# Optimization experiments

Measured on AMD Instinct MI355X. Metric: run time of the kernel, lower is better.

## Reference

```python
import jax, jax.numpy as jnp
import numpy as np

B, C, CI, H, W = 4, 128, 64, 64, 64


def conv1x1(x, w, b):
    # x: [B,C,H,W], w: [Cout,Cin], b: [Cout]
    return jnp.einsum('bchw,oc->bohw', x, w) + b[None, :, None, None]


def setup_inputs() -> dict:
    key = jax.random.key(0)
    ks = jax.random.split(key, 10)
    s = 0.05  # keep logits in a sane range for softmax
    return {
        'x0': jax.random.normal(ks[0], (B, C, H, W), jnp.float32),
        'x1': jax.random.normal(ks[1], (B, C, H, W), jnp.float32),
        'g_w': jax.random.normal(ks[2], (CI, C), jnp.float32) * s,
        'g_b': jax.random.normal(ks[3], (CI,), jnp.float32) * s,
        'theta_w': jax.random.normal(ks[4], (CI, C), jnp.float32) * s,
        'theta_b': jax.random.normal(ks[5], (CI,), jnp.float32) * s,
        'phi_w': jax.random.normal(ks[6], (CI, C), jnp.float32) * s,
        'phi_b': jax.random.normal(ks[7], (CI,), jnp.float32) * s,
        'W_w': jax.random.normal(ks[8], (C, CI), jnp.float32) * s,
        'W_b': jax.random.normal(ks[9], (C,), jnp.float32) * s,
    }


def reference(x0, x1, g_w, g_b, theta_w, theta_b, phi_w, phi_b, W_w, W_b):
    b, c, h, w = x0.shape
    n = h * w
    ci = g_w.shape[0]
    g_x = conv1x1(x0, g_w, g_b).reshape(b, ci, n).transpose(0, 2, 1)      # [B,N,Ci]
    theta_x = conv1x1(x1, theta_w, theta_b).reshape(b, ci, n).transpose(0, 2, 1)  # [B,N,Ci]
    phi_x = conv1x1(x0, phi_w, phi_b).reshape(b, ci, n)                    # [B,Ci,N]
    f = jnp.einsum('bqc,bck->bqk', theta_x, phi_x)                         # [B,N,N]
    f_div_C = jax.nn.softmax(f, axis=-1)
    y = jnp.einsum('bqk,bkc->bqc', f_div_C, g_x)                           # [B,N,Ci]
    y = y.transpose(0, 2, 1).reshape(b, ci, h, w)
    W_y = conv1x1(y, W_w, W_b)
    return W_y + x0
```

## Files before the change

### kernel.cpp

```cpp
#include <hip/hip_runtime.h>
#include <hip/hip_bf16.h>


typedef unsigned int   u32;
typedef unsigned short u16;
typedef __attribute__((ext_vector_type(8))) short short8;
typedef __attribute__((ext_vector_type(4))) short short4v;
typedef __attribute__((ext_vector_type(4))) float f32x4;

#define LOG2E 1.4426950408889634f
#define KSPLIT 8

__device__ __forceinline__ float b2f(u16 v) {
  union { u32 u; float f; } x; x.u = ((u32)v) << 16; return x.f;
}
__device__ __forceinline__ u16 f2b(float f) {
  u32 u = __float_as_uint(f);
  return (u16)((u + 0x8000u) >> 16);
}
__device__ __forceinline__ short8 load_w_frag(const float* p, float s) {
  const float4 f0 = ((const float4*)p)[0];
  const float4 f1 = ((const float4*)p)[1];
  union { u32 w[4]; short8 s8; } r;
  r.w[0] = (u32)f2b(f0.x * s) | ((u32)f2b(f0.y * s) << 16);
  r.w[1] = (u32)f2b(f0.z * s) | ((u32)f2b(f0.w * s) << 16);
  r.w[2] = (u32)f2b(f1.x * s) | ((u32)f2b(f1.y * s) << 16);
  r.w[3] = (u32)f2b(f1.z * s) | ((u32)f2b(f1.w * s) << 16);
  return r.s8;
}


__global__ __launch_bounds__(256) void qkv_fused_kernel(
    const float* __restrict__ x0, const float* __restrict__ x1,
    const float* __restrict__ tw, const float* __restrict__ tb,
    const float* __restrict__ pw, const float* __restrict__ pb,
    const float* __restrict__ gw, const float* __restrict__ gb,
    u16* __restrict__ Q, u16* __restrict__ K, u16* __restrict__ Vt)
{
  const int n0 = blockIdx.x * 64;
  const int b  = blockIdx.y;
  const int t  = threadIdx.x;

  __shared__ __align__(16) short xt[2][64][136];

  #pragma unroll 8
  for (int i = 0; i < 64; ++i) {
    const int idx = i * 256 + t;
    const int tensor = idx >> 13;
    const int c = (idx >> 6) & 127;
    const int n = idx & 63;
    const float v = (tensor ? x1 : x0)[((size_t)b * 128 + c) * 4096 + n0 + n];
    xt[tensor][n][c] = (short)f2b(v);
  }
  asm volatile("" ::: "memory");
  __syncthreads();

  const int wave = t >> 6;
  const int lane = t & 63;
  const int quad = lane >> 4, l15 = lane & 15;

  if (wave < 2) {
    const int conv = wave;
    const float* wsrc = conv ? pw : tw;
    const float  ws   = conv ? 1.f : LOG2E;
    const short* xl   = &xt[conv ? 0 : 1][0][0];

    f32x4 acc[4][4];
    #pragma unroll
    for (int i = 0; i < 4; ++i)
      #pragma unroll
      for (int j = 0; j < 4; ++j) acc[i][j] = (f32x4){0.f, 0.f, 0.f, 0.f};

    #pragma unroll
    for (int kk = 0; kk < 4; ++kk) {
      short8 wf[4], xf[4];
      #pragma unroll
      for (int ot = 0; ot < 4; ++ot)
        wf[ot] = load_w_frag(wsrc + (ot * 16 + l15) * 128 + kk * 32 + quad * 8, ws);
      #pragma unroll
      for (int nt = 0; nt < 4; ++nt)
        xf[nt] = *(const short8*)(xl + (nt * 16 + l15) * 136 + kk * 32 + quad * 8);
      #pragma unroll
      for (int i = 0; i < 4; ++i)
        #pragma unroll
        for (int j = 0; j < 4; ++j)
          acc[i][j] = __builtin_amdgcn_mfma_f32_16x16x32_bf16(xf[i], wf[j], acc[i][j], 0, 0, 0);
    }

    u16* dst = (conv ? K : Q) + (size_t)b * 4096 * 64;
    const float* bias = conv ? pb : tb;
    const float bscale = conv ? 1.f : LOG2E;
    #pragma unroll
    for (int ot = 0; ot < 4; ++ot) {
      const float bv = bias[ot * 16 + l15] * bscale;
      #pragma unroll
      for (int nt = 0; nt < 4; ++nt)
        #pragma unroll
        for (int r = 0; r < 4; ++r) {
          const int n = n0 + nt * 16 + quad * 4 + r;
          dst[(size_t)n * 64 + ot * 16 + l15] = f2b(acc[nt][ot][r] + bv);
        }
    }
  } else {
    const int oh = wave - 2;
    const short* xl = &xt[0][0][0];

    f32x4 acc[2][4];
    #pragma unroll
    for (int i = 0; i < 2; ++i)
      #pragma unroll
      for (int j = 0; j < 4; ++j) acc[i][j] = (f32x4){0.f, 0.f, 0.f, 0.f};

    #pragma unroll
    for (int kk = 0; kk < 4; ++kk) {
      short8 wf[2], xf[4];
      #pragma unroll
      for (int ot = 0; ot < 2; ++ot)
        wf[ot] = load_w_frag(gw + ((oh * 2 + ot) * 16 + l15) * 128 + kk * 32 + quad * 8, 1.f);
      #pragma unroll
      for (int nt = 0; nt < 4; ++nt)
        xf[nt] = *(const short8*)(xl + (nt * 16 + l15) * 136 + kk * 32 + quad * 8);
      #pragma unroll
      for (int i = 0; i < 2; ++i)
        #pragma unroll
        for (int j = 0; j < 4; ++j)
          acc[i][j] = __builtin_amdgcn_mfma_f32_16x16x32_bf16(wf[i], xf[j], acc[i][j], 0, 0, 0);
    }

    u16* dst = Vt + (size_t)b * 64 * 4096;
    #pragma unroll
    for (int ot = 0; ot < 2; ++ot)
      #pragma unroll
      for (int r = 0; r < 4; ++r) {
        const int o = (oh * 2 + ot) * 16 + quad * 4 + r;
        const float bv = gb[o];
        #pragma unroll
        for (int nc = 0; nc < 4; ++nc)
          dst[(size_t)o * 4096 + n0 + nc * 16 + l15] = f2b(acc[ot][nc][r] + bv);
      }
  }
}

__global__ __launch_bounds__(256) void attn_kernel(
    const u16* __restrict__ Q, const u16* __restrict__ K,
    const u16* __restrict__ Vt, u16* __restrict__ Opart,
    float* __restrict__ Lp)
{
  const int qt = blockIdx.x, b = blockIdx.y, ks = blockIdx.z;
  const int tid  = threadIdx.x;
  const int wave = tid >> 6;
  const int lane = tid & 63;
  const int quad = lane >> 4;
  const int l15  = lane & 15;

  __shared__ __align__(16) short P_lds[4][64][72];
  short* pw = &P_lds[wave][0][0];

  const int q0 = qt * 256 + wave * 64;
  const u16* Qb = Q  + (size_t)b * 4096 * 64;
  const u16* Kb = K  + (size_t)b * 4096 * 64;
  const u16* Vb = Vt + (size_t)b * 64 * 4096;

  short8 qf[4][2];
  #pragma unroll
  for (int nt = 0; nt < 4; ++nt) {
    const u16* qp = Qb + (size_t)(q0 + nt * 16 + l15) * 64 + quad * 8;
    qf[nt][0] = *(const short8*)qp;
    qf[nt][1] = *(const short8*)(qp + 32);
  }

  f32x4 oacc[4][4];
  #pragma unroll
  for (int i = 0; i < 4; ++i)
    #pragma unroll
    for (int j = 0; j < 4; ++j)
      oacc[i][j] = (f32x4){0.f, 0.f, 0.f, 0.f};
  float lsum[4] = {0.f, 0.f, 0.f, 0.f};

  const int kbase = ks * (4096 / KSPLIT);
  const int NKT   = 4096 / KSPLIT / 64;

  short8 kf[4][2];
  #pragma unroll
  for (int mt = 0; mt < 4; ++mt) {
    const u16* kp = Kb + (size_t)(kbase + mt * 16 + l15) * 64 + quad * 8;
    kf[mt][0] = *(const short8*)kp;
    kf[mt][1] = *(const short8*)(kp + 32);
  }

  for (int kt = 0; kt < NKT; ++kt) {
    const int k0 = kbase + kt * 64;

    short8 vf[4][2];
    #pragma unroll
    for (int nd = 0; nd < 4; ++nd) {
      const u16* vp = Vb + (size_t)(nd * 16 + l15) * 4096 + k0 + quad * 8;
      vf[nd][0] = *(const short8*)vp;
      vf[nd][1] = *(const short8*)(vp + 32);
    }

    #pragma unroll
    for (int mt = 0; mt < 4; ++mt) {
      #pragma unroll
      for (int nt = 0; nt < 4; ++nt) {
        f32x4 s = {0.f, 0.f, 0.f, 0.f};
        s = __builtin_amdgcn_mfma_f32_16x16x32_bf16(kf[mt][0], qf[nt][0], s, 0, 0, 0);
        s = __builtin_amdgcn_mfma_f32_16x16x32_bf16(kf[mt][1], qf[nt][1], s, 0, 0, 0);
        float p0 = exp2f(s[0]), p1 = exp2f(s[1]), p2 = exp2f(s[2]), p3 = exp2f(s[3]);
        lsum[nt] += (p0 + p1) + (p2 + p3);
        u32 u0 = __float_as_uint(p0) + 0x8000u;
        u32 u1 = __float_as_uint(p1) + 0x8000u;
        u32 u2 = __float_as_uint(p2) + 0x8000u;
        u32 u3 = __float_as_uint(p3) + 0x8000u;
        union { uint2 u; short4v s4; } pk;
        pk.u.x = __builtin_amdgcn_perm(u1, u0, 0x07060302u);
        pk.u.y = __builtin_amdgcn_perm(u3, u2, 0x07060302u);
        *(short4v*)(pw + (nt * 16 + l15) * 72 + mt * 16 + quad * 4) = pk.s4;
      }
    }

    if (kt < NKT - 1) {
      #pragma unroll
      for (int mt = 0; mt < 4; ++mt) {
        const u16* kp = Kb + (size_t)(k0 + 64 + mt * 16 + l15) * 64 + quad * 8;
        kf[mt][0] = *(const short8*)kp;
        kf[mt][1] = *(const short8*)(kp + 32);
      }
    }

    asm volatile("" ::: "memory");

    #pragma unroll
    for (int mq = 0; mq < 4; ++mq) {
      const short* pr = pw + (mq * 16 + l15) * 72 + quad * 8;
      short8 pa0 = *(const short8*)pr;
      short8 pa1 = *(const short8*)(pr + 32);
      #pragma unroll
      for (int nd = 0; nd < 4; ++nd) {
        oacc[mq][nd] = __builtin_amdgcn_mfma_f32_16x16x32_bf16(pa0, vf[nd][0], oacc[mq][nd], 0, 0, 0);
        oacc[mq][nd] = __builtin_amdgcn_mfma_f32_16x16x32_bf16(pa1, vf[nd][1], oacc[mq][nd], 0, 0, 0);
      }
    }

    asm volatile("" ::: "memory");
  }

  #pragma unroll
  for (int nt = 0; nt < 4; ++nt) {
    float v = lsum[nt];
    v += __shfl_xor(v, 16, 64);
    v += __shfl_xor(v, 32, 64);
    lsum[nt] = v;
  }
  float* LpB = Lp + ((size_t)ks * 4 + b) * 4096;
  if (quad == 0) {
    #pragma unroll
    for (int nt = 0; nt < 4; ++nt)
      LpB[q0 + nt * 16 + l15] = lsum[nt];
  }

  u16* Ob = Opart + ((size_t)ks * 4 + b) * 4096 * 64;
  #pragma unroll
  for (int mq = 0; mq < 4; ++mq)
    #pragma unroll
    for (int nd = 0; nd < 4; ++nd)
      #pragma unroll
      for (int r = 0; r < 4; ++r) {
        int q = q0 + mq * 16 + quad * 4 + r;
        Ob[(size_t)q * 64 + nd * 16 + l15] = f2b(oacc[mq][nd][r]);
      }
}

__global__ __launch_bounds__(256) void out_fused_kernel(
    const u16* __restrict__ Opart, const float* __restrict__ Lp,
    const float* __restrict__ Wf, const float* __restrict__ Wbf,
    const float* __restrict__ x0, float* __restrict__ out)
{
  const int n0 = blockIdx.x * 64;
  const int b  = blockIdx.y;
  const int t  = threadIdx.x;

  __shared__ __align__(16) short Ys[64][72];

  {
    const int nl = t >> 2;
    const int q4 = t & 3;
    const int ng = n0 + nl;

    float l = 0.f;
    #pragma unroll
    for (int ks = 0; ks < KSPLIT; ++ks)
      l += Lp[((size_t)ks * 4 + b) * 4096 + ng];

    float a[16];
    #pragma unroll
    for (int j = 0; j < 16; ++j) a[j] = 0.f;
    #pragma unroll
    for (int ks = 0; ks < KSPLIT; ++ks) {
      const uint4* row = (const uint4*)(Opart + (((size_t)ks * 4 + b) * 4096 + ng) * 64 + q4 * 16);
      #pragma unroll
      for (int v = 0; v < 2; ++v) {
        uint4 r = row[v];
        u32 wds[4] = {r.x, r.y, r.z, r.w};
        #pragma unroll
        for (int j = 0; j < 4; ++j) {
          a[v * 8 + 2 * j]     += __uint_as_float(wds[j] << 16);
          a[v * 8 + 2 * j + 1] += __uint_as_float(wds[j] & 0xffff0000u);
        }
      }
    }
    const float rinv = 1.f / l;
    union { u32 w[8]; short8 s8[2]; } pk;
    #pragma unroll
    for (int j = 0; j < 8; ++j)
      pk.w[j] = (u32)f2b(a[2 * j] * rinv) | ((u32)f2b(a[2 * j + 1] * rinv) << 16);
    *(short8*)&Ys[nl][q4 * 16]     = pk.s8[0];
    *(short8*)&Ys[nl][q4 * 16 + 8] = pk.s8[1];
  }
  asm volatile("" ::: "memory");
  __syncthreads();

  const int wave = t >> 6;
  const int lane = t & 63;
  const int quad = lane >> 4, l15 = lane & 15;

  f32x4 acc[2][4];
  #pragma unroll
  for (int i = 0; i < 2; ++i)
    #pragma unroll
    for (int j = 0; j < 4; ++j) acc[i][j] = (f32x4){0.f, 0.f, 0.f, 0.f};

  #pragma unroll
  for (int kk = 0; kk < 2; ++kk) {
    short8 wf[2], yf[4];
    #pragma unroll
    for (int ot = 0; ot < 2; ++ot)
      wf[ot] = load_w_frag(Wf + ((wave * 2 + ot) * 16 + l15) * 64 + kk * 32 + quad * 8, 1.f);
    #pragma unroll
    for (int nt = 0; nt < 4; ++nt)
      yf[nt] = *(const short8*)&Ys[nt * 16 + l15][kk * 32 + quad * 8];
    #pragma unroll
    for (int i = 0; i < 2; ++i)
      #pragma unroll
      for (int j = 0; j < 4; ++j)
        acc[i][j] = __builtin_amdgcn_mfma_f32_16x16x32_bf16(wf[i], yf[j], acc[i][j], 0, 0, 0);
  }

  #pragma unroll
  for (int ot = 0; ot < 2; ++ot)
    #pragma unroll
    for (int r = 0; r < 4; ++r) {
      const int o = (wave * 2 + ot) * 16 + quad * 4 + r;
      const float bv = Wbf[o];
      #pragma unroll
      for (int nt = 0; nt < 4; ++nt) {
        const size_t idx = ((size_t)(b * 128 + o)) * 4096 + n0 + nt * 16 + l15;
        out[idx] = acc[ot][nt][r] + bv + x0[idx];
      }
    }
}

extern "C" void kernel_launch(void* const* d_in, const int* in_sizes, int n_in,
                              void* d_out, int out_size, void* d_ws, size_t ws_size,
                              hipStream_t stream) {
  const float* x0 = (const float*)d_in[0];
  const float* x1 = (const float*)d_in[1];
  const float* gw = (const float*)d_in[2];
  const float* gb = (const float*)d_in[3];
  const float* tw = (const float*)d_in[4];
  const float* tb = (const float*)d_in[5];
  const float* pw = (const float*)d_in[6];
  const float* pb = (const float*)d_in[7];
  const float* Ww = (const float*)d_in[8];
  const float* Wb = (const float*)d_in[9];
  float* out = (float*)d_out;

  char* ws = (char*)d_ws;
  u16*   Qw    = (u16*)(ws + 0);
  u16*   Kw    = (u16*)(ws + (2u << 20));
  u16*   Vtw   = (u16*)(ws + (4u << 20));
  u16*   Opart = (u16*)(ws + (6u << 20));
  float* Lp    = (float*)(ws + (22u << 20));

  qkv_fused_kernel<<<dim3(64, 4), dim3(256), 0, stream>>>(
      x0, x1, tw, tb, pw, pb, gw, gb, Qw, Kw, Vtw);

  attn_kernel<<<dim3(16, 4, KSPLIT), dim3(256), 0, stream>>>(Qw, Kw, Vtw, Opart, Lp);

  out_fused_kernel<<<dim3(64, 4), dim3(256), 0, stream>>>(
      Opart, Lp, Ww, Wb, x0, out);
}
```

Measured before the change: 136.0 us.

## Fuse three kernels into one persistent kernel with grid barriers

Merges the QKV projection, split-K attention and output projection kernels into a single 512-block launch separated by two software grid barriers built on atomic counters. Blocks 0-255 do the projection phases and all 512 do attention, with the LDS buffer reused across phases. This removes two kernel launch gaps and the tail drain between stages. In exchange it adds a memset launch, spin-wait barriers, and a reliance on all 512 blocks being co-resident, which launch_bounds(256,2) is meant to ensure.

```diff
diff --git a/kernel.cpp b/kernel.cpp
--- a/kernel.cpp
+++ b/kernel.cpp
@@ -29,335 +29,338 @@
   return r.s8;
 }
 
-
-__global__ __launch_bounds__(256) void qkv_fused_kernel(
+__device__ __forceinline__ void grid_barrier(u32* cnt, u32 target) {
+  __syncthreads();
+  if (threadIdx.x == 0) {
+    __builtin_amdgcn_fence(__ATOMIC_RELEASE, "agent");
+    __hip_atomic_fetch_add(cnt, 1u, __ATOMIC_RELAXED, __HIP_MEMORY_SCOPE_AGENT);
+    while (__hip_atomic_load(cnt, __ATOMIC_RELAXED, __HIP_MEMORY_SCOPE_AGENT) < target) {
+      __builtin_amdgcn_s_sleep(2);
+    }
+    __builtin_amdgcn_fence(__ATOMIC_ACQUIRE, "agent");
+  }
+  __syncthreads();
+}
+
+
+__global__ __launch_bounds__(256, 2) void fused_all_kernel(
     const float* __restrict__ x0, const float* __restrict__ x1,
     const float* __restrict__ tw, const float* __restrict__ tb,
     const float* __restrict__ pw, const float* __restrict__ pb,
     const float* __restrict__ gw, const float* __restrict__ gb,
-    u16* __restrict__ Q, u16* __restrict__ K, u16* __restrict__ Vt)
+    const float* __restrict__ Wf, const float* __restrict__ Wbf,
+    float* __restrict__ out,
+    u16* __restrict__ Q, u16* __restrict__ K, u16* __restrict__ Vt,
+    u16* __restrict__ Opart, float* __restrict__ Lp, u32* __restrict__ bar)
 {
-  const int n0 = blockIdx.x * 64;
-  const int b  = blockIdx.y;
-  const int t  = threadIdx.x;
-
-  __shared__ __align__(16) short xt[2][64][136];
-
-  #pragma unroll 8
-  for (int i = 0; i < 64; ++i) {
-    const int idx = i * 256 + t;
-    const int tensor = idx >> 13;
-    const int c = (idx >> 6) & 127;
-    const int n = idx & 63;
-    const float v = (tensor ? x1 : x0)[((size_t)b * 128 + c) * 4096 + n0 + n];
-    xt[tensor][n][c] = (short)f2b(v);
-  }
-  asm volatile("" ::: "memory");
-  __syncthreads();
-
+  __shared__ __align__(16) char smem[4 * 64 * 72 * 2];
+
+  const int bid  = blockIdx.x;
+  const int t    = threadIdx.x;
   const int wave = t >> 6;
   const int lane = t & 63;
   const int quad = lane >> 4, l15 = lane & 15;
 
-  if (wave < 2) {
-    const int conv = wave;
-    const float* wsrc = conv ? pw : tw;
-    const float  ws   = conv ? 1.f : LOG2E;
-    const short* xl   = &xt[conv ? 0 : 1][0][0];
-
-    f32x4 acc[4][4];
+  if (bid < 256) {
+    const int n0 = (bid & 63) * 64;
+    const int b  = bid >> 6;
+    auto xt = (short (*)[64][136])smem;
+
+    #pragma unroll 8
+    for (int i = 0; i < 64; ++i) {
+      const int idx = i * 256 + t;
+      const int tensor = idx >> 13;
+      const int c = (idx >> 6) & 127;
+      const int n = idx & 63;
+      const float v = (tensor ? x1 : x0)[((size_t)b * 128 + c) * 4096 + n0 + n];
+      xt[tensor][n][c] = (short)f2b(v);
+    }
+    asm volatile("" ::: "memory");
+    __syncthreads();
+
+    if (wave < 2) {
+      const int conv = wave;
+      const float* wsrc = conv ? pw : tw;
+      const float  ws   = conv ? 1.f : LOG2E;
+      const short* xl   = &xt[conv ? 0 : 1][0][0];
+
+      f32x4 acc[4][4];
+      #pragma unroll
+      for (int i = 0; i < 4; ++i)
+        #pragma unroll
+        for (int j = 0; j < 4; ++j) acc[i][j] = (f32x4){0.f, 0.f, 0.f, 0.f};
+
+      #pragma unroll
+      for (int kk = 0; kk < 4; ++kk) {
+        short8 wf[4], xf[4];
+        #pragma unroll
+        for (int ot = 0; ot < 4; ++ot)
+          wf[ot] = load_w_frag(wsrc + (ot * 16 + l15) * 128 + kk * 32 + quad * 8, ws);
+        #pragma unroll
+        for (int nt = 0; nt < 4; ++nt)
+          xf[nt] = *(const short8*)(xl + (nt * 16 + l15) * 136 + kk * 32 + quad * 8);
+        #pragma unroll
+        for (int i = 0; i < 4; ++i)
+          #pragma unroll
+          for (int j = 0; j < 4; ++j)
+            acc[i][j] = __builtin_amdgcn_mfma_f32_16x16x32_bf16(xf[i], wf[j], acc[i][j], 0, 0, 0);
+      }
+
+      u16* dst = (conv ? K : Q) + (size_t)b * 4096 * 64;
+      const float* bias = conv ? pb : tb;
+      const float bscale = conv ? 1.f : LOG2E;
+      #pragma unroll
+      for (int ot = 0; ot < 4; ++ot) {
+        const float bv = bias[ot * 16 + l15] * bscale;
+        #pragma unroll
+        for (int nt = 0; nt < 4; ++nt)
+          #pragma unroll
+          for (int r = 0; r < 4; ++r) {
+            const int n = n0 + nt * 16 + quad * 4 + r;
+            dst[(size_t)n * 64 + ot * 16 + l15] = f2b(acc[nt][ot][r] + bv);
+          }
+      }
+    } else {
+      const int oh = wave - 2;
+      const short* xl = &xt[0][0][0];
+
+      f32x4 acc[2][4];
+      #pragma unroll
+      for (int i = 0; i < 2; ++i)
+        #pragma unroll
+        for (int j = 0; j < 4; ++j) acc[i][j] = (f32x4){0.f, 0.f, 0.f, 0.f};
+
+      #pragma unroll
+      for (int kk = 0; kk < 4; ++kk) {
+        short8 wf[2], xf[4];
+        #pragma unroll
+        for (int ot = 0; ot < 2; ++ot)
+          wf[ot] = load_w_frag(gw + ((oh * 2 + ot) * 16 + l15) * 128 + kk * 32 + quad * 8, 1.f);
+        #pragma unroll
+        for (int nt = 0; nt < 4; ++nt)
+          xf[nt] = *(const short8*)(xl + (nt * 16 + l15) * 136 + kk * 32 + quad * 8);
+        #pragma unroll
+        for (int i = 0; i < 2; ++i)
+          #pragma unroll
+          for (int j = 0; j < 4; ++j)
+            acc[i][j] = __builtin_amdgcn_mfma_f32_16x16x32_bf16(wf[i], xf[j], acc[i][j], 0, 0, 0);
+      }
+
+      u16* dst = Vt + (size_t)b * 64 * 4096;
+      #pragma unroll
+      for (int ot = 0; ot < 2; ++ot)
+        #pragma unroll
+        for (int r = 0; r < 4; ++r) {
+          const int o = (oh * 2 + ot) * 16 + quad * 4 + r;
+          const float bv = gb[o];
+          #pragma unroll
+          for (int nc = 0; nc < 4; ++nc)
+            dst[(size_t)o * 4096 + n0 + nc * 16 + l15] = f2b(acc[ot][nc][r] + bv);
+        }
+    }
+  }
+
+  grid_barrier(bar + 0, 512);
+
+  {
+    const int qt = bid & 15, b = (bid >> 4) & 3, ks = bid >> 6;
+    short* pl = (short*)smem + wave * 64 * 72;
+
+    const int q0 = qt * 256 + wave * 64;
+    const u16* Qb = Q  + (size_t)b * 4096 * 64;
+    const u16* Kb = K  + (size_t)b * 4096 * 64;
+    const u16* Vb = Vt + (size_t)b * 64 * 4096;
+
+    short8 qf[4][2];
+    #pragma unroll
+    for (int nt = 0; nt < 4; ++nt) {
+      const u16* qp = Qb + (size_t)(q0 + nt * 16 + l15) * 64 + quad * 8;
+      qf[nt][0] = *(const short8*)qp;
+      qf[nt][1] = *(const short8*)(qp + 32);
+    }
+
+    f32x4 oacc[4][4];
     #pragma unroll
     for (int i = 0; i < 4; ++i)
       #pragma unroll
+      for (int j = 0; j < 4; ++j)
+        oacc[i][j] = (f32x4){0.f, 0.f, 0.f, 0.f};
+    float lsum[4] = {0.f, 0.f, 0.f, 0.f};
+
+    const int kbase = ks * (4096 / KSPLIT);
+    const int NKT   = 4096 / KSPLIT / 64;
+
+    short8 kf[4][2];
+    #pragma unroll
+    for (int mt = 0; mt < 4; ++mt) {
+      const u16* kp = Kb + (size_t)(kbase + mt * 16 + l15) * 64 + quad * 8;
+      kf[mt][0] = *(const short8*)kp;
+      kf[mt][1] = *(const short8*)(kp + 32);
+    }
+
+    for (int kt = 0; kt < NKT; ++kt) {
+      const int k0 = kbase + kt * 64;
+
+      short8 vf[4][2];
+      #pragma unroll
+      for (int nd = 0; nd < 4; ++nd) {
+        const u16* vp = Vb + (size_t)(nd * 16 + l15) * 4096 + k0 + quad * 8;
+        vf[nd][0] = *(const short8*)vp;
+        vf[nd][1] = *(const short8*)(vp + 32);
+      }
+
+      #pragma unroll
+      for (int mt = 0; mt < 4; ++mt) {
+        #pragma unroll
+        for (int nt = 0; nt < 4; ++nt) {
+          f32x4 s = {0.f, 0.f, 0.f, 0.f};
+          s = __builtin_amdgcn_mfma_f32_16x16x32_bf16(kf[mt][0], qf[nt][0], s, 0, 0, 0);
+          s = __builtin_amdgcn_mfma_f32_16x16x32_bf16(kf[mt][1], qf[nt][1], s, 0, 0, 0);
+          float p0 = exp2f(s[0]), p1 = exp2f(s[1]), p2 = exp2f(s[2]), p3 = exp2f(s[3]);
+          lsum[nt] += (p0 + p1) + (p2 + p3);
+          u32 u0 = __float_as_uint(p0) + 0x8000u;
+          u32 u1 = __float_as_uint(p1) + 0x8000u;
+          u32 u2 = __float_as_uint(p2) + 0x8000u;
+          u32 u3 = __float_as_uint(p3) + 0x8000u;
+          union { uint2 u; short4v s4; } pk;
+          pk.u.x = __builtin_amdgcn_perm(u1, u0, 0x07060302u);
+          pk.u.y = __builtin_amdgcn_perm(u3, u2, 0x07060302u);
+          *(short4v*)(pl + (nt * 16 + l15) * 72 + mt * 16 + quad * 4) = pk.s4;
+        }
+      }
+
+      if (kt < NKT - 1) {
+        #pragma unroll
+        for (int mt = 0; mt < 4; ++mt) {
+          const u16* kp = Kb + (size_t)(k0 + 64 + mt * 16 + l15) * 64 + quad * 8;
+          kf[mt][0] = *(const short8*)kp;
+          kf[mt][1] = *(const short8*)(kp + 32);
+        }
+      }
+
+      asm volatile("" ::: "memory");
+
+      #pragma unroll
+      for (int mq = 0; mq < 4; ++mq) {
+        const short* pr = pl + (mq * 16 + l15) * 72 + quad * 8;
+        short8 pa0 = *(const short8*)pr;
+        short8 pa1 = *(const short8*)(pr + 32);
+        #pragma unroll
+        for (int nd = 0; nd < 4; ++nd) {
+          oacc[mq][nd] = __builtin_amdgcn_mfma_f32_16x16x32_bf16(pa0, vf[nd][0], oacc[mq][nd], 0, 0, 0);
+          oacc[mq][nd] = __builtin_amdgcn_mfma_f32_16x16x32_bf16(pa1, vf[nd][1], oacc[mq][nd], 0, 0, 0);
+        }
+      }
+
+      asm volatile("" ::: "memory");
+    }
+
+    #pragma unroll
+    for (int nt = 0; nt < 4; ++nt) {
+      float v = lsum[nt];
+      v += __shfl_xor(v, 16, 64);
+      v += __shfl_xor(v, 32, 64);
+      lsum[nt] = v;
+    }
+    float* LpB = Lp + ((size_t)ks * 4 + b) * 4096;
+    if (quad == 0) {
+      #pragma unroll
+      for (int nt = 0; nt < 4; ++nt)
+        LpB[q0 + nt * 16 + l15] = lsum[nt];
+    }
+
+    u16* Ob = Opart + ((size_t)ks * 4 + b) * 4096 * 64;
+    #pragma unroll
+    for (int mq = 0; mq < 4; ++mq)
+      #pragma unroll
+      for (int nd = 0; nd < 4; ++nd)
+        #pragma unroll
+        for (int r = 0; r < 4; ++r) {
+          const int q = q0 + mq * 16 + quad * 4 + r;
+          Ob[(size_t)q * 64 + nd * 16 + l15] = f2b(oacc[mq][nd][r]);
+        }
+  }
+
+  grid_barrier(bar + 1, 512);
+
+  if (bid < 256) {
+    const int n0 = (bid & 63) * 64;
+    const int b  = bid >> 6;
+    auto Ys = (short (*)[72])smem;
+
+    {
+      const int nl = t >> 2;
+      const int q4 = t & 3;
+      const int ng = n0 + nl;
+
+      float l = 0.f;
+      #pragma unroll
+      for (int ks = 0; ks < KSPLIT; ++ks)
+        l += Lp[((size_t)ks * 4 + b) * 4096 + ng];
+
+      float a[16];
+      #pragma unroll
+      for (int j = 0; j < 16; ++j) a[j] = 0.f;
+      #pragma unroll
+      for (int ks = 0; ks < KSPLIT; ++ks) {
+        const uint4* row = (const uint4*)(Opart + (((size_t)ks * 4 + b) * 4096 + ng) * 64 + q4 * 16);
+        #pragma unroll
+        for (int v = 0; v < 2; ++v) {
+          uint4 r = row[v];
+          u32 wds[4] = {r.x, r.y, r.z, r.w};
+          #pragma unroll
+          for (int j = 0; j < 4; ++j) {
+            a[v * 8 + 2 * j]     += __uint_as_float(wds[j] << 16);
+            a[v * 8 + 2 * j + 1] += __uint_as_float(wds[j] & 0xffff0000u);
+          }
+        }
+      }
+      const float rinv = 1.f / l;
+      union { u32 w[8]; short8 s8[2]; } pk;
+      #pragma unroll
+      for (int j = 0; j < 8; ++j)
+        pk.w[j] = (u32)f2b(a[2 * j] * rinv) | ((u32)f2b(a[2 * j + 1] * rinv) << 16);
+      *(short8*)&Ys[nl][q4 * 16]     = pk.s8[0];
+      *(short8*)&Ys[nl][q4 * 16 + 8] = pk.s8[1];
+    }
+    asm volatile("" ::: "memory");
+    __syncthreads();
+
+    f32x4 acc[2][4];
+    #pragma unroll
+    for (int i = 0; i < 2; ++i)
+      #pragma unroll
       for (int j = 0; j < 4; ++j) acc[i][j] = (f32x4){0.f, 0.f, 0.f, 0.f};
 
     #pragma unroll
-    for (int kk = 0; kk < 4; ++kk) {
-      short8 wf[4], xf[4];
-      #pragma unroll
-      for (int ot = 0; ot < 4; ++ot)
-        wf[ot] = load_w_frag(wsrc + (ot * 16 + l15) * 128 + kk * 32 + quad * 8, ws);
+    for (int kk = 0; kk < 2; ++kk) {
+      short8 wf[2], yf[4];
+      #pragma unroll
+      for (int ot = 0; ot < 2; ++ot)
+        wf[ot] = load_w_frag(Wf + ((wave * 2 + ot) * 16 + l15) * 64 + kk * 32 + quad * 8, 1.f);
       #pragma unroll
       for (int nt = 0; nt < 4; ++nt)
-        xf[nt] = *(const short8*)(xl + (nt * 16 + l15) * 136 + kk * 32 + quad * 8);
-      #pragma unroll
-      for (int i = 0; i < 4; ++i)
+        yf[nt] = *(const short8*)&Ys[nt * 16 + l15][kk * 32 + quad * 8];
+      #pragma unroll
+      for (int i = 0; i < 2; ++i)
         #pragma unroll
         for (int j = 0; j < 4; ++j)
-          acc[i][j] = __builtin_amdgcn_mfma_f32_16x16x32_bf16(xf[i], wf[j], acc[i][j], 0, 0, 0);
-    }
-
-    u16* dst = (conv ? K : Q) + (size_t)b * 4096 * 64;
-    const float* bias = conv ? pb : tb;
-    const float bscale = conv ? 1.f : LOG2E;
-    #pragma unroll
-    for (int ot = 0; ot < 4; ++ot) {
-      const float bv = bias[ot * 16 + l15] * bscale;
-      #pragma unroll
-      for (int nt = 0; nt < 4; ++nt)
-        #pragma unroll
-        for (int r = 0; r < 4; ++r) {
-          const int n = n0 + nt * 16 + quad * 4 + r;
-          dst[(size_t)n * 64 + ot * 16 + l15] = f2b(acc[nt][ot][r] + bv);
-        }
-    }
-  } else {
-    const int oh = wave - 2;
-    const short* xl = &xt[0][0][0];
-
-    f32x4 acc[2][4];
-    #pragma unroll
-    for (int i = 0; i < 2; ++i)
-      #pragma unroll
-      for (int j = 0; j < 4; ++j) acc[i][j] = (f32x4){0.f, 0.f, 0.f, 0.f};
-
-    #pragma unroll
-    for (int kk = 0; kk < 4; ++kk) {
-      short8 wf[2], xf[4];
-      #pragma unroll
-      for (int ot = 0; ot < 2; ++ot)
-        wf[ot] = load_w_frag(gw + ((oh * 2 + ot) * 16 + l15) * 128 + kk * 32 + quad * 8, 1.f);
-      #pragma unroll
-      for (int nt = 0; nt < 4; ++nt)
-        xf[nt] = *(const short8*)(xl + (nt * 16 + l15) * 136 + kk * 32 + quad * 8);
-      #pragma unroll
-      for (int i = 0; i < 2; ++i)
-        #pragma unroll
-        for (int j = 0; j < 4; ++j)
-          acc[i][j] = __builtin_amdgcn_mfma_f32_16x16x32_bf16(wf[i], xf[j], acc[i][j], 0, 0, 0);
-    }
-
-    u16* dst = Vt + (size_t)b * 64 * 4096;
+          acc[i][j] = __builtin_amdgcn_mfma_f32_16x16x32_bf16(wf[i], yf[j], acc[i][j], 0, 0, 0);
+    }
+
     #pragma unroll
     for (int ot = 0; ot < 2; ++ot)
       #pragma unroll
       for (int r = 0; r < 4; ++r) {
-        const int o = (oh * 2 + ot) * 16 + quad * 4 + r;
-        const float bv = gb[o];
-        #pragma unroll
-        for (int nc = 0; nc < 4; ++nc)
-          dst[(size_t)o * 4096 + n0 + nc * 16 + l15] = f2b(acc[ot][nc][r] + bv);
+        const int o = (wave * 2 + ot) * 16 + quad * 4 + r;
+        const float bv = Wbf[o];
+        #pragma unroll
+        for (int nt = 0; nt < 4; ++nt) {
+          const size_t idx = ((size_t)(b * 128 + o)) * 4096 + n0 + nt * 16 + l15;
+          out[idx] = acc[ot][nt][r] + bv + x0[idx];
+        }
       }
   }
-}
-
-__global__ __launch_bounds__(256) void attn_kernel(
-    const u16* __restrict__ Q, const u16* __restrict__ K,
-    const u16* __restrict__ Vt, u16* __restrict__ Opart,
-    float* __restrict__ Lp)
-{
-  const int qt = blockIdx.x, b = blockIdx.y, ks = blockIdx.z;
-  const int tid  = threadIdx.x;
-  const int wave = tid >> 6;
-  const int lane = tid & 63;
-  const int quad = lane >> 4;
-  const int l15  = lane & 15;
-
-  __shared__ __align__(16) short P_lds[4][64][72];
-  short* pw = &P_lds[wave][0][0];
-
-  const int q0 = qt * 256 + wave * 64;
-  const u16* Qb = Q  + (size_t)b * 4096 * 64;
-  const u16* Kb = K  + (size_t)b * 4096 * 64;
-  const u16* Vb = Vt + (size_t)b * 64 * 4096;
-
-  short8 qf[4][2];
-  #pragma unroll
-  for (int nt = 0; nt < 4; ++nt) {
-    const u16* qp = Qb + (size_t)(q0 + nt * 16 + l15) * 64 + quad * 8;
-    qf[nt][0] = *(const short8*)qp;
-    qf[nt][1] = *(const short8*)(qp + 32);
-  }
-
-  f32x4 oacc[4][4];
-  #pragma unroll
-  for (int i = 0; i < 4; ++i)
-    #pragma unroll
-    for (int j = 0; j < 4; ++j)
-      oacc[i][j] = (f32x4){0.f, 0.f, 0.f, 0.f};
-  float lsum[4] = {0.f, 0.f, 0.f, 0.f};
-
-  const int kbase = ks * (4096 / KSPLIT);
-  const int NKT   = 4096 / KSPLIT / 64;
-
-  short8 kf[4][2];
-  #pragma unroll
-  for (int mt = 0; mt < 4; ++mt) {
-    const u16* kp = Kb + (size_t)(kbase + mt * 16 + l15) * 64 + quad * 8;
-    kf[mt][0] = *(const short8*)kp;
-    kf[mt][1] = *(const short8*)(kp + 32);
-  }
-
-  for (int kt = 0; kt < NKT; ++kt) {
-    const int k0 = kbase + kt * 64;
-
-    short8 vf[4][2];
-    #pragma unroll
-    for (int nd = 0; nd < 4; ++nd) {
-      const u16* vp = Vb + (size_t)(nd * 16 + l15) * 4096 + k0 + quad * 8;
-      vf[nd][0] = *(const short8*)vp;
-      vf[nd][1] = *(const short8*)(vp + 32);
-    }
-
-    #pragma unroll
-    for (int mt = 0; mt < 4; ++mt) {
-      #pragma unroll
-      for (int nt = 0; nt < 4; ++nt) {
-        f32x4 s = {0.f, 0.f, 0.f, 0.f};
-        s = __builtin_amdgcn_mfma_f32_16x16x32_bf16(kf[mt][0], qf[nt][0], s, 0, 0, 0);
-        s = __builtin_amdgcn_mfma_f32_16x16x32_bf16(kf[mt][1], qf[nt][1], s, 0, 0, 0);
-        float p0 = exp2f(s[0]), p1 = exp2f(s[1]), p2 = exp2f(s[2]), p3 = exp2f(s[3]);
-        lsum[nt] += (p0 + p1) + (p2 + p3);
-        u32 u0 = __float_as_uint(p0) + 0x8000u;
-        u32 u1 = __float_as_uint(p1) + 0x8000u;
-        u32 u2 = __float_as_uint(p2) + 0x8000u;
-        u32 u3 = __float_as_uint(p3) + 0x8000u;
-        union { uint2 u; short4v s4; } pk;
-        pk.u.x = __builtin_amdgcn_perm(u1, u0, 0x07060302u);
-        pk.u.y = __builtin_amdgcn_perm(u3, u2, 0x07060302u);
-        *(short4v*)(pw + (nt * 16 + l15) * 72 + mt * 16 + quad * 4) = pk.s4;
-      }
-    }
-
-    if (kt < NKT - 1) {
-      #pragma unroll
-      for (int mt = 0; mt < 4; ++mt) {
-        const u16* kp = Kb + (size_t)(k0 + 64 + mt * 16 + l15) * 64 + quad * 8;
-        kf[mt][0] = *(const short8*)kp;
-        kf[mt][1] = *(const short8*)(kp + 32);
-      }
-    }
-
-    asm volatile("" ::: "memory");
-
-    #pragma unroll
-    for (int mq = 0; mq < 4; ++mq) {
-      const short* pr = pw + (mq * 16 + l15) * 72 + quad * 8;
-      short8 pa0 = *(const short8*)pr;
-      short8 pa1 = *(const short8*)(pr + 32);
-      #pragma unroll
-      for (int nd = 0; nd < 4; ++nd) {
-        oacc[mq][nd] = __builtin_amdgcn_mfma_f32_16x16x32_bf16(pa0, vf[nd][0], oacc[mq][nd], 0, 0, 0);
-        oacc[mq][nd] = __builtin_amdgcn_mfma_f32_16x16x32_bf16(pa1, vf[nd][1], oacc[mq][nd], 0, 0, 0);
-      }
-    }
-
-    asm volatile("" ::: "memory");
-  }
-
-  #pragma unroll
-  for (int nt = 0; nt < 4; ++nt) {
-    float v = lsum[nt];
-    v += __shfl_xor(v, 16, 64);
-    v += __shfl_xor(v, 32, 64);
-    lsum[nt] = v;
-  }
-  float* LpB = Lp + ((size_t)ks * 4 + b) * 4096;
-  if (quad == 0) {
-    #pragma unroll
-    for (int nt = 0; nt < 4; ++nt)
-      LpB[q0 + nt * 16 + l15] = lsum[nt];
-  }
-
-  u16* Ob = Opart + ((size_t)ks * 4 + b) * 4096 * 64;
-  #pragma unroll
-  for (int mq = 0; mq < 4; ++mq)
-    #pragma unroll
-    for (int nd = 0; nd < 4; ++nd)
-      #pragma unroll
-      for (int r = 0; r < 4; ++r) {
-        int q = q0 + mq * 16 + quad * 4 + r;
-        Ob[(size_t)q * 64 + nd * 16 + l15] = f2b(oacc[mq][nd][r]);
-      }
-}
-
-__global__ __launch_bounds__(256) void out_fused_kernel(
-    const u16* __restrict__ Opart, const float* __restrict__ Lp,
-    const float* __restrict__ Wf, const float* __restrict__ Wbf,
-    const float* __restrict__ x0, float* __restrict__ out)
-{
-  const int n0 = blockIdx.x * 64;
-  const int b  = blockIdx.y;
-  const int t  = threadIdx.x;
-
-  __shared__ __align__(16) short Ys[64][72];
-
-  {
-    const int nl = t >> 2;
-    const int q4 = t & 3;
-    const int ng = n0 + nl;
-
-    float l = 0.f;
-    #pragma unroll
-    for (int ks = 0; ks < KSPLIT; ++ks)
-      l += Lp[((size_t)ks * 4 + b) * 4096 + ng];
-
-    float a[16];
-    #pragma unroll
-    for (int j = 0; j < 16; ++j) a[j] = 0.f;
-    #pragma unroll
-    for (int ks = 0; ks < KSPLIT; ++ks) {
-      const uint4* row = (const uint4*)(Opart + (((size_t)ks * 4 + b) * 4096 + ng) * 64 + q4 * 16);
-      #pragma unroll
-      for (int v = 0; v < 2; ++v) {
-        uint4 r = row[v];
-        u32 wds[4] = {r.x, r.y, r.z, r.w};
-        #pragma unroll
-        for (int j = 0; j < 4; ++j) {
-          a[v * 8 + 2 * j]     += __uint_as_float(wds[j] << 16);
-          a[v * 8 + 2 * j + 1] += __uint_as_float(wds[j] & 0xffff0000u);
-        }
-      }
-    }
-    const float rinv = 1.f / l;
-    union { u32 w[8]; short8 s8[2]; } pk;
-    #pragma unroll
-    for (int j = 0; j < 8; ++j)
-      pk.w[j] = (u32)f2b(a[2 * j] * rinv) | ((u32)f2b(a[2 * j + 1] * rinv) << 16);
-    *(short8*)&Ys[nl][q4 * 16]     = pk.s8[0];
-    *(short8*)&Ys[nl][q4 * 16 + 8] = pk.s8[1];
-  }
-  asm volatile("" ::: "memory");
-  __syncthreads();
-
-  const int wave = t >> 6;
-  const int lane = t & 63;
-  const int quad = lane >> 4, l15 = lane & 15;
-
-  f32x4 acc[2][4];
-  #pragma unroll
-  for (int i = 0; i < 2; ++i)
-    #pragma unroll
-    for (int j = 0; j < 4; ++j) acc[i][j] = (f32x4){0.f, 0.f, 0.f, 0.f};
-
-  #pragma unroll
-  for (int kk = 0; kk < 2; ++kk) {
-    short8 wf[2], yf[4];
-    #pragma unroll
-    for (int ot = 0; ot < 2; ++ot)
-      wf[ot] = load_w_frag(Wf + ((wave * 2 + ot) * 16 + l15) * 64 + kk * 32 + quad * 8, 1.f);
-    #pragma unroll
-    for (int nt = 0; nt < 4; ++nt)
-      yf[nt] = *(const short8*)&Ys[nt * 16 + l15][kk * 32 + quad * 8];
-    #pragma unroll
-    for (int i = 0; i < 2; ++i)
-      #pragma unroll
-      for (int j = 0; j < 4; ++j)
-        acc[i][j] = __builtin_amdgcn_mfma_f32_16x16x32_bf16(wf[i], yf[j], acc[i][j], 0, 0, 0);
-  }
-
-  #pragma unroll
-  for (int ot = 0; ot < 2; ++ot)
-    #pragma unroll
-    for (int r = 0; r < 4; ++r) {
-      const int o = (wave * 2 + ot) * 16 + quad * 4 + r;
-      const float bv = Wbf[o];
-      #pragma unroll
-      for (int nt = 0; nt < 4; ++nt) {
-        const size_t idx = ((size_t)(b * 128 + o)) * 4096 + n0 + nt * 16 + l15;
-        out[idx] = acc[ot][nt][r] + bv + x0[idx];
-      }
-    }
 }
 
 extern "C" void kernel_launch(void* const* d_in, const int* in_sizes, int n_in,
@@ -381,12 +384,11 @@
   u16*   Vtw   = (u16*)(ws + (4u << 20));
   u16*   Opart = (u16*)(ws + (6u << 20));
   float* Lp    = (float*)(ws + (22u << 20));
-
-  qkv_fused_kernel<<<dim3(64, 4), dim3(256), 0, stream>>>(
-      x0, x1, tw, tb, pw, pb, gw, gb, Qw, Kw, Vtw);
-
-  attn_kernel<<<dim3(16, 4, KSPLIT), dim3(256), 0, stream>>>(Qw, Kw, Vtw, Opart, Lp);
-
-  out_fused_kernel<<<dim3(64, 4), dim3(256), 0, stream>>>(
-      Opart, Lp, Ww, Wb, x0, out);
-}
+  u32*   bar   = (u32*)(ws + (23u << 20));
+
+  hipMemsetAsync(bar, 0, 2 * sizeof(u32), stream);
+
+  fused_all_kernel<<<dim3(512), dim3(256), 0, stream>>>(
+      x0, x1, tw, tb, pw, pb, gw, gb, Ww, Wb, out,
+      Qw, Kw, Vtw, Opart, Lp, bar);
+}
```

Result: slower. 214.9 us (+58.0%).
